# Kernel optimization log

Hardware: AMD Instinct MI355X
Metric: run time of the kernel (lower is better)

The kernel has to match this reference:

```python
import jax, jax.numpy as jnp
import numpy as np

L, H, C, V, T_BLK = 12, 12, 768, 50257, 1024
D = C // H  # head dim = 64


def _layernorm(x, g, b, eps=1e-5):
    m = jnp.mean(x, axis=-1, keepdims=True)
    v = jnp.mean(jnp.square(x - m), axis=-1, keepdims=True)
    return (x - m) * jax.lax.rsqrt(v + eps) * g + b


def setup_inputs() -> dict:
    key = jax.random.key(0)
    ks = jax.random.split(key, 8)
    B, T = 8, 1024
    s = 0.02
    sp = 0.02 / np.sqrt(2 * L)  # c_proj special init
    return {
        "idx": jax.random.randint(ks[0], (B, T), 0, V, dtype=jnp.int32),
        "wte": jax.random.normal(ks[1], (V, C), jnp.float32) * s,
        "wpe": jax.random.normal(ks[2], (T_BLK, C), jnp.float32) * s,
        "ln1_g": jnp.ones((L, C), jnp.float32),
        "ln1_b": jnp.zeros((L, C), jnp.float32),
        "w_qkv": jax.random.normal(ks[3], (L, C, 3 * C), jnp.float32) * s,
        "b_qkv": jnp.zeros((L, 3 * C), jnp.float32),
        "w_ao": jax.random.normal(ks[4], (L, C, C), jnp.float32) * sp,
        "b_ao": jnp.zeros((L, C), jnp.float32),
        "ln2_g": jnp.ones((L, C), jnp.float32),
        "ln2_b": jnp.zeros((L, C), jnp.float32),
        "w_fc": jax.random.normal(ks[5], (L, C, 4 * C), jnp.float32) * s,
        "b_fc": jnp.zeros((L, 4 * C), jnp.float32),
        "w_mo": jax.random.normal(ks[6], (L, 4 * C, C), jnp.float32) * sp,
        "b_mo": jnp.zeros((L, C), jnp.float32),
        "lnf_g": jnp.ones((C,), jnp.float32),
        "lnf_b": jnp.zeros((C,), jnp.float32),
    }


def reference(idx, wte, wpe, ln1_g, ln1_b, w_qkv, b_qkv, w_ao, b_ao,
              ln2_g, ln2_b, w_fc, b_fc, w_mo, b_mo, lnf_g, lnf_b):
    B, T = idx.shape
    scale = 1.0 / np.sqrt(D)
    causal = jnp.tril(jnp.ones((T, T), dtype=bool))  # [T,T]

    x = wte[idx] + wpe[:T]  # [B,T,C]

    def block(x, p):
        g1, b1, wq, bq, wo, bo, g2, b2_, wf, bf, w2, b2m = p
        h = _layernorm(x, g1, b1)
        qkv = h @ wq + bq  # [B,T,3C]
        q, k, v = jnp.split(qkv, 3, axis=-1)
        q = q.reshape(B, T, H, D)
        k = k.reshape(B, T, H, D)
        v = v.reshape(B, T, H, D)
        att = jnp.einsum('bqhd,bkhd->bhqk', q, k) * scale
        att = jnp.where(causal, att, -jnp.inf)
        att = jax.nn.softmax(att, axis=-1)
        y = jnp.einsum('bhqk,bkhd->bqhd', att, v).reshape(B, T, C)
        x = x + y @ wo + bo
        h2 = _layernorm(x, g2, b2_)
        x = x + jax.nn.gelu(h2 @ wf + bf, approximate=False) @ w2 + b2m
        return x, None

    params = (ln1_g, ln1_b, w_qkv, b_qkv, w_ao, b_ao,
              ln2_g, ln2_b, w_fc, b_fc, w_mo, b_mo)
    x, _ = jax.lax.scan(block, x, params)

    x = _layernorm(x, lnf_g, lnf_b)
    # inference path: logits only for last position, lm_head tied to wte
    logits = x[:, -1:, :] @ wte.T  # [B,1,V]
    return logits
```

## Files before the change

### kernel.cpp

```cpp
#include <hip/hip_runtime.h>

#define B_ 8
#define T_ 1024
#define C_ 768
#define H_ 12
#define L_ 12
#define V_ 50257

typedef __bf16 bf16_t;
typedef __bf16 bf16x8 __attribute__((ext_vector_type(8)));
typedef __bf16 bf16x4 __attribute__((ext_vector_type(4)));
typedef float f32x4 __attribute__((ext_vector_type(4)));

#define AS1 __attribute__((address_space(1)))
#define AS3 __attribute__((address_space(3)))

__device__ __forceinline__ unsigned short f2bf(float f) {
  bf16_t h = (bf16_t)f;
  return __builtin_bit_cast(unsigned short, h);
}

__device__ __forceinline__ unsigned short bfbits(bf16_t h) {
  return __builtin_bit_cast(unsigned short, h);
}

template<int CTRL>
__device__ __forceinline__ float dppf(float x) {
  return __builtin_bit_cast(float, __builtin_amdgcn_update_dpp(
      0, __builtin_bit_cast(int, x), CTRL, 0xF, 0xF, true));
}
__device__ __forceinline__ float red16_max(float x) {
  x = fmaxf(x, dppf<0xB1>(x));
  x = fmaxf(x, dppf<0x4E>(x));
  x = fmaxf(x, dppf<0x124>(x));
  x = fmaxf(x, dppf<0x128>(x));
  return x;
}
__device__ __forceinline__ float red16_sum(float x) {
  x += dppf<0xB1>(x);
  x += dppf<0x4E>(x);
  x += dppf<0x124>(x);
  x += dppf<0x128>(x);
  return x;
}

__global__ __launch_bounds__(192) void embed_kernel(
    const int* __restrict__ idx, const float* __restrict__ wte,
    const float* __restrict__ wpe, float* __restrict__ xf)
{
  const int bt = blockIdx.x;
  const int t = bt & (T_ - 1);
  const int tok = idx[bt];
  const int c4 = threadIdx.x << 2;
  float4 a = *(const float4*)(wte + (size_t)tok * C_ + c4);
  float4 p = *(const float4*)(wpe + (size_t)t * C_ + c4);
  float4 r; r.x = a.x + p.x; r.y = a.y + p.y; r.z = a.z + p.z; r.w = a.w + p.w;
  *(float4*)(xf + (size_t)bt * C_ + c4) = r;
}

template<bool LAST>
__global__ __launch_bounds__(256) void ln_kernel(
    const float* __restrict__ x, const float* __restrict__ gw,
    const float* __restrict__ bw, unsigned short* __restrict__ obf,
    float* __restrict__ of)
{
  __shared__ float red[8];
  const size_t row = LAST ? ((size_t)blockIdx.x * T_ + (T_ - 1)) : (size_t)blockIdx.x;
  const float* xr = x + row * C_;
  const int t = threadIdx.x;
  float v0 = xr[t], v1 = xr[t + 256], v2 = xr[t + 512];
  float s = v0 + v1 + v2;
  #pragma unroll
  for (int off = 32; off; off >>= 1) s += __shfl_xor(s, off);
  if ((t & 63) == 0) red[t >> 6] = s;
  __syncthreads();
  const float mean = (red[0] + red[1] + red[2] + red[3]) * (1.0f / C_);
  const float d0 = v0 - mean, d1 = v1 - mean, d2 = v2 - mean;
  float ss = d0 * d0 + d1 * d1 + d2 * d2;
  #pragma unroll
  for (int off = 32; off; off >>= 1) ss += __shfl_xor(ss, off);
  if ((t & 63) == 0) red[4 + (t >> 6)] = ss;
  __syncthreads();
  const float var = (red[4] + red[5] + red[6] + red[7]) * (1.0f / C_);
  const float rs = rsqrtf(var + 1e-5f);
  float o0 = d0 * rs * gw[t] + bw[t];
  float o1 = d1 * rs * gw[t + 256] + bw[t + 256];
  float o2 = d2 * rs * gw[t + 512] + bw[t + 512];
  if (LAST) {
    float* orow = of + (size_t)blockIdx.x * C_;
    orow[t] = o0; orow[t + 256] = o1; orow[t + 512] = o2;
  } else {
    unsigned short* orow = obf + row * C_;
    orow[t] = f2bf(o0); orow[t + 256] = f2bf(o1); orow[t + 512] = f2bf(o2);
  }
}

__global__ __launch_bounds__(256) void cvtw4_kernel(
    const float* __restrict__ wq, const float* __restrict__ wa,
    const float* __restrict__ wf, const float* __restrict__ wm,
    unsigned short* __restrict__ out)
{
  __shared__ float tile[32][33];
  const int i = blockIdx.x;
  const float* W; unsigned short* Wt; int K, N, tix;
  if (i < 1728)      { W = wq; Wt = out;                 K = C_;     N = 3 * C_; tix = i; }
  else if (i < 2304) { W = wa; Wt = out + 3 * C_ * C_;   K = C_;     N = C_;     tix = i - 1728; }
  else if (i < 4608) { W = wf; Wt = out + 4 * C_ * C_;   K = C_;     N = 4 * C_; tix = i - 2304; }
  else               { W = wm; Wt = out + 8 * C_ * C_;   K = 4 * C_; N = C_;     tix = i - 4608; }
  const int ntx = N >> 5;
  const int kb = (tix / ntx) << 5, nb = (tix % ntx) << 5;
  const int t = threadIdx.x;
  {
    const int k = t >> 3, n4 = (t & 7) << 2;
    float4 v = *(const float4*)(W + (size_t)(kb + k) * N + nb + n4);
    tile[k][n4] = v.x; tile[k][n4 + 1] = v.y; tile[k][n4 + 2] = v.z; tile[k][n4 + 3] = v.w;
  }
  __syncthreads();
  {
    const int n = t >> 3, k4 = (t & 7) << 2;
    ushort4 o;
    o.x = f2bf(tile[k4][n]);     o.y = f2bf(tile[k4 + 1][n]);
    o.z = f2bf(tile[k4 + 2][n]); o.w = f2bf(tile[k4 + 3][n]);
    *(ushort4*)(Wt + (size_t)(nb + n) * K + kb + k4) = o;
  }
}

template<int EPI>
__global__ __launch_bounds__(512, 1) void gemm256(
    const unsigned short* __restrict__ A, const unsigned short* __restrict__ Bt,
    const float* __restrict__ bias, unsigned short* __restrict__ Cb,
    int N, int K, int nx)
{
  __shared__ __align__(16) unsigned short As[2][2][128 * 64];
  __shared__ __align__(16) unsigned short Bs[2][2][128 * 64];
  const int tid = threadIdx.x;
  const int lane = tid & 63;
  const int w = tid >> 6;
  const int wr = w >> 2;
  const int wc = w & 3;
  const int l15 = lane & 15, l4 = lane >> 4;
  const int s7 = l15 & 7;

  const int bid = blockIdx.x;
  const int xcd = bid & 7;
  const int j = bid >> 3;
  const int mblk = xcd * 4 + j / nx;
  const int nblk = j - (j / nx) * nx;
  const int m0 = mblk * 256, n0 = nblk * 256;

  f32x4 acc[8][4] = {};

  const int srow8 = lane >> 3;
  const int sch = (lane & 7) ^ srow8;

  auto stageA = [&](int h, int kt, int q) {
    const size_t k0 = (size_t)kt * 64;
    #pragma unroll
    for (int jj = 0; jj < 2; ++jj)
      __builtin_amdgcn_global_load_lds(
          (const AS1 unsigned int*)(A + (size_t)(m0 + h * 128 + jj * 64 + w * 8 + srow8) * K + sch * 8 + k0),
          (AS3 unsigned int*)(&As[q][h][(jj * 8 + w) * 512]), 16, 0, 0);
  };
  auto stageB = [&](int h, int kt, int q) {
    const size_t k0 = (size_t)kt * 64;
    #pragma unroll
    for (int jj = 0; jj < 2; ++jj)
      __builtin_amdgcn_global_load_lds(
          (const AS1 unsigned int*)(Bt + (size_t)(n0 + h * 128 + jj * 64 + w * 8 + srow8) * K + sch * 8 + k0),
          (AS3 unsigned int*)(&Bs[q][h][(jj * 8 + w) * 512]), 16, 0, 0);
  };

  const int nk = K >> 6;
  stageA(0, 0, 0); stageA(1, 0, 0); stageB(0, 0, 0); stageB(1, 0, 0);

  for (int t = 0; t < nk; ++t) {
    const int p = t & 1, q = p ^ 1;
    const bool pf = (t + 1 < nk);
    bf16x8 Af[4][2], Bf[2][2];
    auto rdA = [&](int f, int ks) -> bf16x8 {
      return *(const bf16x8*)(&As[p][wr][(f * 16 + l15) * 64 + ((((ks << 2) | l4) ^ s7) << 3)]);
    };
    auto rdB = [&](int nf, int ks) -> bf16x8 {
      return *(const bf16x8*)(&Bs[p][wc >> 1][((wc & 1) * 64 + nf * 16 + l15) * 64 + ((((ks << 2) | l4) ^ s7) << 3)]);
    };

    if (pf) { stageA(0, t + 1, q); asm volatile("s_waitcnt vmcnt(2)" ::: "memory"); }
    else    { asm volatile("s_waitcnt vmcnt(0)" ::: "memory"); }
    __builtin_amdgcn_s_barrier();
    #pragma unroll
    for (int f = 0; f < 4; ++f) { Af[f][0] = rdA(f, 0); Af[f][1] = rdA(f, 1); }
    #pragma unroll
    for (int nf = 0; nf < 2; ++nf) { Bf[nf][0] = rdB(nf, 0); Bf[nf][1] = rdB(nf, 1); }
    asm volatile("s_waitcnt lgkmcnt(0)" ::: "memory");
    __builtin_amdgcn_sched_barrier(0);
    __builtin_amdgcn_s_setprio(1);
    #pragma unroll
    for (int f = 0; f < 4; ++f)
      #pragma unroll
      for (int nf = 0; nf < 2; ++nf)
        #pragma unroll
        for (int ks = 0; ks < 2; ++ks)
          acc[f][nf] = __builtin_amdgcn_mfma_f32_16x16x32_bf16(Af[f][ks], Bf[nf][ks], acc[f][nf], 0, 0, 0);
    __builtin_amdgcn_s_setprio(0);
    __builtin_amdgcn_s_barrier();

    if (pf) stageA(1, t + 1, q);
    #pragma unroll
    for (int nf = 0; nf < 2; ++nf) { Bf[nf][0] = rdB(nf + 2, 0); Bf[nf][1] = rdB(nf + 2, 1); }
    __builtin_amdgcn_s_barrier();
    asm volatile("s_waitcnt lgkmcnt(0)" ::: "memory");
    __builtin_amdgcn_sched_barrier(0);
    __builtin_amdgcn_s_setprio(1);
    #pragma unroll
    for (int f = 0; f < 4; ++f)
      #pragma unroll
      for (int nf = 0; nf < 2; ++nf)
        #pragma unroll
        for (int ks = 0; ks < 2; ++ks)
          acc[f][nf + 2] = __builtin_amdgcn_mfma_f32_16x16x32_bf16(Af[f][ks], Bf[nf][ks], acc[f][nf + 2], 0, 0, 0);
    __builtin_amdgcn_s_setprio(0);
    __builtin_amdgcn_s_barrier();

    if (pf) stageB(0, t + 1, q);
    #pragma unroll
    for (int f = 0; f < 4; ++f) { Af[f][0] = rdA(f + 4, 0); Af[f][1] = rdA(f + 4, 1); }
    __builtin_amdgcn_s_barrier();
    asm volatile("s_waitcnt lgkmcnt(0)" ::: "memory");
    __builtin_amdgcn_sched_barrier(0);
    __builtin_amdgcn_s_setprio(1);
    #pragma unroll
    for (int f = 0; f < 4; ++f)
      #pragma unroll
      for (int nf = 0; nf < 2; ++nf)
        #pragma unroll
        for (int ks = 0; ks < 2; ++ks)
          acc[f + 4][nf + 2] = __builtin_amdgcn_mfma_f32_16x16x32_bf16(Af[f][ks], Bf[nf][ks], acc[f + 4][nf + 2], 0, 0, 0);
    __builtin_amdgcn_s_setprio(0);
    __builtin_amdgcn_s_barrier();

    if (pf) stageB(1, t + 1, q);
    #pragma unroll
    for (int nf = 0; nf < 2; ++nf) { Bf[nf][0] = rdB(nf, 0); Bf[nf][1] = rdB(nf, 1); }
    __builtin_amdgcn_s_barrier();
    asm volatile("s_waitcnt lgkmcnt(0)" ::: "memory");
    __builtin_amdgcn_sched_barrier(0);
    __builtin_amdgcn_s_setprio(1);
    #pragma unroll
    for (int f = 0; f < 4; ++f)
      #pragma unroll
      for (int nf = 0; nf < 2; ++nf)
        #pragma unroll
        for (int ks = 0; ks < 2; ++ks)
          acc[f + 4][nf] = __builtin_amdgcn_mfma_f32_16x16x32_bf16(Af[f][ks], Bf[nf][ks], acc[f + 4][nf], 0, 0, 0);
    __builtin_amdgcn_s_setprio(0);
    __builtin_amdgcn_s_barrier();
  }

  #pragma unroll
  for (int f = 0; f < 8; ++f) {
    #pragma unroll
    for (int nf = 0; nf < 4; ++nf) {
      const int col = n0 + wc * 64 + nf * 16 + l15;
      const float bv = bias[col];
      int hh = 0, dd = 0;
      unsigned short* qkvo = nullptr;
      if constexpr (EPI == 3) {
        const int which = col / C_;
        const int rem = col - which * C_;
        hh = rem >> 6; dd = rem & 63;
        qkvo = Cb + (size_t)which * ((size_t)B_ * H_ * T_ * 64);
      }
      #pragma unroll
      for (int i = 0; i < 4; ++i) {
        const int row = mblk * 256 + wr * 128 + f * 16 + l4 * 4 + i;
        float v = acc[f][nf][i] + bv;
        if constexpr (EPI == 2) {
          float g = 0.5f * v * (1.0f + erff(v * 0.70710678118f));
          Cb[(size_t)row * N + col] = f2bf(g);
        } else {
          const int bb = row >> 10, tt = row & (T_ - 1);
          qkvo[(((size_t)bb * H_ + hh) * T_ + tt) * 64 + dd] = f2bf(v);
        }
      }
    }
  }
}

template<int EPI>
__global__ __launch_bounds__(256, 2) void gemm_bt(
    const unsigned short* __restrict__ A, const unsigned short* __restrict__ Bt,
    const float* __restrict__ bias, float* __restrict__ Cf,
    unsigned short* __restrict__ Cb, int M, int N, int K, int nx)
{
  (void)M;
  __shared__ unsigned short As[2][128 * 64];
  __shared__ unsigned short Bs[2][128 * 64];
  const int tid = threadIdx.x;
  const int lane = tid & 63;
  const int w = tid >> 6;
  const int wr = w >> 1, wc = w & 1;
  const int l15 = lane & 15, l4 = lane >> 4;
  const int swz = lane & 7;

  const int bid = blockIdx.x;
  const int xcd = bid & 7;
  const int j = bid >> 3;
  const int mblk = xcd * 8 + j / nx;
  const int nblk = j - (j / nx) * nx;
  const int m0 = mblk * 128, n0 = nblk * 128;

  f32x4 acc[4][4] = {};

  const int srow = lane >> 3;
  const int schunk = (lane & 7) ^ srow;
  const unsigned short* aSrc = A + (size_t)(m0 + w * 32 + srow) * K + schunk * 8;
  const unsigned short* bSrc = Bt + (size_t)(n0 + w * 32 + srow) * K + schunk * 8;
  const int ldsRowBase = (w * 32) * 64;

  auto stage = [&](int kt, int p) {
    const int k0 = kt << 6;
    #pragma unroll
    for (int jj = 0; jj < 4; ++jj)
      __builtin_amdgcn_global_load_lds(
          (const AS1 unsigned int*)(aSrc + (size_t)jj * 8 * K + k0),
          (AS3 unsigned int*)(&As[p][ldsRowBase + jj * 8 * 64]), 16, 0, 0);
    #pragma unroll
    for (int jj = 0; jj < 4; ++jj)
      __builtin_amdgcn_global_load_lds(
          (const AS1 unsigned int*)(bSrc + (size_t)jj * 8 * K + k0),
          (AS3 unsigned int*)(&Bs[p][ldsRowBase + jj * 8 * 64]), 16, 0, 0);
  };

  auto compute = [&](int p) {
    const unsigned short* aw = &As[p][(wr * 64) * 64];
    const unsigned short* bw2 = &Bs[p][(wc * 64) * 64];
    #pragma unroll
    for (int ks = 0; ks < 2; ++ks) {
      bf16x8 af[4], bf[4];
      #pragma unroll
      for (int mf = 0; mf < 4; ++mf)
        af[mf] = *(const bf16x8*)(aw + (mf * 16 + l15) * 64 + (((ks << 2) | l4) ^ swz) * 8);
      #pragma unroll
      for (int nf = 0; nf < 4; ++nf)
        bf[nf] = *(const bf16x8*)(bw2 + (nf * 16 + l15) * 64 + (((ks << 2) | l4) ^ swz) * 8);
      __builtin_amdgcn_s_setprio(1);
      #pragma unroll
      for (int mf = 0; mf < 4; ++mf)
        #pragma unroll
        for (int nf = 0; nf < 4; ++nf)
          acc[mf][nf] = __builtin_amdgcn_mfma_f32_16x16x32_bf16(af[mf], bf[nf], acc[mf][nf], 0, 0, 0);
      __builtin_amdgcn_s_setprio(0);
    }
  };

  const int nk = K >> 6;
  stage(0, 0);
  for (int kt = 0; kt < nk - 1; ++kt) {
    const int p = kt & 1;
    stage(kt + 1, p ^ 1);
    asm volatile("s_waitcnt vmcnt(8)" ::: "memory");
    __builtin_amdgcn_s_barrier();
    compute(p);
    __builtin_amdgcn_s_barrier();
  }
  asm volatile("s_waitcnt vmcnt(0)" ::: "memory");
  __builtin_amdgcn_s_barrier();
  compute((nk - 1) & 1);

  #pragma unroll
  for (int mf = 0; mf < 4; ++mf) {
    #pragma unroll
    for (int nf = 0; nf < 4; ++nf) {
      const int col = n0 + wc * 64 + nf * 16 + l15;
      const float bv = bias[col];
      #pragma unroll
      for (int i = 0; i < 4; ++i) {
        const int row = m0 + wr * 64 + mf * 16 + l4 * 4 + i;
        float v = acc[mf][nf][i] + bv;
        if constexpr (EPI == 1) {
          Cf[(size_t)row * N + col] += v;
        } else if constexpr (EPI == 2) {
          float g = 0.5f * v * (1.0f + erff(v * 0.70710678118f));
          Cb[(size_t)row * N + col] = f2bf(g);
        }
      }
    }
  }
}

__global__ __launch_bounds__(256) void attn_kernel(
    const unsigned short* __restrict__ Qb, const unsigned short* __restrict__ Kb,
    const unsigned short* __restrict__ Vb, unsigned short* __restrict__ y)
{
  const int pb = blockIdx.x / 96;
  const int bh = blockIdx.x % 96;
  const int h = bh % H_;
  const int b = bh / H_;
  const int tid = threadIdx.x, lane = tid & 63, w = tid >> 6;
  const int l15 = lane & 15, l4 = lane >> 4;

  const int qw = (w < 2) ? (pb * 64 + w * 32) : ((15 - pb) * 64 + (w - 2) * 32);
  const int NT = (17 - pb) >> 1;

  __shared__ unsigned short Ks[128 * 64];
  __shared__ unsigned short Vt[64 * 136];
  __shared__ unsigned short Pb[4][32 * 74];

  const unsigned short* qp = Qb + ((size_t)bh * T_ + qw) * 64;
  bf16x8 qf[2][2];
  #pragma unroll
  for (int mf = 0; mf < 2; ++mf)
    #pragma unroll
    for (int ks = 0; ks < 2; ++ks)
      qf[mf][ks] = *(const bf16x8*)(qp + (mf * 16 + l15) * 64 + ks * 32 + l4 * 8);

  f32x4 o[2][4] = {};
  float mrow[2][4], lrow[2][4];
  #pragma unroll
  for (int mf = 0; mf < 2; ++mf)
    #pragma unroll
    for (int i = 0; i < 4; ++i) { mrow[mf][i] = -1e30f; lrow[mf][i] = 0.0f; }

  const unsigned short* kb0 = Kb + (size_t)bh * T_ * 64;
  const unsigned short* vb0 = Vb + (size_t)bh * T_ * 64;
  const int ck = w;
  const int skey = lane;
  const int sw = (skey & 7);

  bf16x8 kr0, kr1, kr2, kr3, vr0, vr1, vr2, vr3;
  {
    const unsigned short* kp = kb0 + (size_t)skey * 64;
    const unsigned short* vp = vb0 + (size_t)skey * 64;
    kr0 = *(const bf16x8*)(kp + ck * 8);
    kr1 = *(const bf16x8*)(kp + (ck + 4) * 8);
    kr2 = *(const bf16x8*)(kp + 64 * 64 + ck * 8);
    kr3 = *(const bf16x8*)(kp + 64 * 64 + (ck + 4) * 8);
    vr0 = *(const bf16x8*)(vp + ck * 8);
    vr1 = *(const bf16x8*)(vp + (ck + 4) * 8);
    vr2 = *(const bf16x8*)(vp + 64 * 64 + ck * 8);
    vr3 = *(const bf16x8*)(vp + 64 * 64 + (ck + 4) * 8);
  }

  for (int kt = 0; kt < NT; ++kt) {
    const int k0 = kt << 7;
    __syncthreads();
    *(bf16x8*)(Ks + skey * 64 + ((ck ^ sw) * 8)) = kr0;
    *(bf16x8*)(Ks + skey * 64 + (((ck + 4) ^ sw) * 8)) = kr1;
    *(bf16x8*)(Ks + (skey + 64) * 64 + ((ck ^ sw) * 8)) = kr2;
    *(bf16x8*)(Ks + (skey + 64) * 64 + (((ck + 4) ^ sw) * 8)) = kr3;
    #pragma unroll
    for (int jj = 0; jj < 8; ++jj) {
      Vt[(ck * 8 + jj) * 136 + skey]            = bfbits(vr0[jj]);
      Vt[((ck + 4) * 8 + jj) * 136 + skey]      = bfbits(vr1[jj]);
      Vt[(ck * 8 + jj) * 136 + skey + 64]       = bfbits(vr2[jj]);
      Vt[((ck + 4) * 8 + jj) * 136 + skey + 64] = bfbits(vr3[jj]);
    }
    __syncthreads();
    if (kt + 1 < NT) {
      const int kn = (kt + 1) << 7;
      const unsigned short* kp = kb0 + (size_t)(kn + skey) * 64;
      const unsigned short* vp = vb0 + (size_t)(kn + skey) * 64;
      kr0 = *(const bf16x8*)(kp + ck * 8);
      kr1 = *(const bf16x8*)(kp + (ck + 4) * 8);
      kr2 = *(const bf16x8*)(kp + 64 * 64 + ck * 8);
      kr3 = *(const bf16x8*)(kp + 64 * 64 + (ck + 4) * 8);
      vr0 = *(const bf16x8*)(vp + ck * 8);
      vr1 = *(const bf16x8*)(vp + (ck + 4) * 8);
      vr2 = *(const bf16x8*)(vp + 64 * 64 + ck * 8);
      vr3 = *(const bf16x8*)(vp + 64 * 64 + (ck + 4) * 8);
    }

    #pragma unroll
    for (int h2 = 0; h2 < 2; ++h2) {
      const int kh0 = k0 + h2 * 64;
      if (kh0 > qw + 31) continue;

      f32x4 s[2][4] = {};
      __builtin_amdgcn_s_setprio(1);
      #pragma unroll
      for (int ks = 0; ks < 2; ++ks) {
        #pragma unroll
        for (int nfk = 0; nfk < 4; ++nfk) {
          const int key = h2 * 64 + nfk * 16 + l15;
          bf16x8 kf = *(const bf16x8*)(Ks + key * 64 + ((((ks << 2) | l4) ^ (l15 & 7)) * 8));
          #pragma unroll
          for (int mf = 0; mf < 2; ++mf)
            s[mf][nfk] = __builtin_amdgcn_mfma_f32_16x16x32_bf16(qf[mf][ks], kf, s[mf][nfk], 0, 0, 0);
        }
      }
      __builtin_amdgcn_s_setprio(0);

      #pragma unroll
      for (int mf = 0; mf < 2; ++mf) {
        const int qrow = qw + mf * 16 + l4 * 4;
        const bool fullt = (kh0 + 63) <= (qw + mf * 16);
        float pvv[4][4], tm[4];
        #pragma unroll
        for (int i = 0; i < 4; ++i) {
          const int q = qrow + i;
          float m_ = -1e30f;
          #pragma unroll
          for (int nfk = 0; nfk < 4; ++nfk) {
            float x = s[mf][nfk][i] * 0.125f;
            x = fullt ? x : ((kh0 + nfk * 16 + l15 <= q) ? x : -1e30f);
            pvv[nfk][i] = x;
            m_ = fmaxf(m_, x);
          }
          tm[i] = red16_max(m_);
        }
        bool need = false;
        #pragma unroll
        for (int i = 0; i < 4; ++i) need |= (tm[i] > mrow[mf][i] + 8.0f);
        if (__any(need)) {
          #pragma unroll
          for (int i = 0; i < 4; ++i) {
            const float mnew = fmaxf(mrow[mf][i], tm[i]);
            const float alpha = __expf(mrow[mf][i] - mnew);
            mrow[mf][i] = mnew;
            lrow[mf][i] *= alpha;
            #pragma unroll
            for (int nf = 0; nf < 4; ++nf) o[mf][nf][i] *= alpha;
          }
        }
        #pragma unroll
        for (int i = 0; i < 4; ++i) {
          float rsum = 0.0f;
          #pragma unroll
          for (int nfk = 0; nfk < 4; ++nfk) {
            const float p = __expf(pvv[nfk][i] - mrow[mf][i]);
            pvv[nfk][i] = p; rsum += p;
          }
          rsum = red16_sum(rsum);
          lrow[mf][i] += rsum;
        }
        #pragma unroll
        for (int nfk = 0; nfk < 4; ++nfk)
          #pragma unroll
          for (int i = 0; i < 4; ++i)
            Pb[w][(mf * 16 + l4 * 4 + i) * 74 + nfk * 16 + l15] = f2bf(pvv[nfk][i]);
      }

      bf16x8 pa[2][2];
      #pragma unroll
      for (int mf = 0; mf < 2; ++mf)
        #pragma unroll
        for (int k2 = 0; k2 < 2; ++k2)
          pa[mf][k2] = *(const bf16x8*)(Pb[w] + (mf * 16 + l15) * 74 + k2 * 32 + l4 * 8);
      __builtin_amdgcn_s_setprio(1);
      #pragma unroll
      for (int nf = 0; nf < 4; ++nf) {
        const int d = nf * 16 + l15;
        #pragma unroll
        for (int k2 = 0; k2 < 2; ++k2) {
          bf16x8 vf = *(const bf16x8*)(Vt + d * 136 + h2 * 64 + k2 * 32 + l4 * 8);
          #pragma unroll
          for (int mf = 0; mf < 2; ++mf)
            o[mf][nf] = __builtin_amdgcn_mfma_f32_16x16x32_bf16(pa[mf][k2], vf, o[mf][nf], 0, 0, 0);
        }
      }
      __builtin_amdgcn_s_setprio(0);
    }
  }

  #pragma unroll
  for (int mf = 0; mf < 2; ++mf) {
    #pragma unroll
    for (int i = 0; i < 4; ++i) {
      const float inv = 1.0f / lrow[mf][i];
      const int q = qw + mf * 16 + l4 * 4 + i;
      unsigned short* yr = y + (size_t)(b * T_ + q) * C_ + h * 64;
      #pragma unroll
      for (int nf = 0; nf < 4; ++nf)
        yr[nf * 16 + l15] = f2bf(o[mf][nf][i] * inv);
    }
  }
}

__global__ __launch_bounds__(256) void head_kernel(
    const float* __restrict__ lnf, const float* __restrict__ wte,
    float* __restrict__ out)
{
  __shared__ float xs[B_ * C_];
  for (int i = threadIdx.x; i < B_ * C_; i += 256) xs[i] = lnf[i];
  __syncthreads();
  const int w = threadIdx.x >> 6, lane = threadIdx.x & 63;
  const int v = blockIdx.x * 4 + w;
  if (v >= V_) return;
  const float* wv = wte + (size_t)v * C_ + lane * 12;
  float4 w0 = *(const float4*)(wv);
  float4 w1 = *(const float4*)(wv + 4);
  float4 w2 = *(const float4*)(wv + 8);
  float acc[B_];
  #pragma unroll
  for (int bb = 0; bb < B_; ++bb) {
    const float* xr = xs + bb * C_ + lane * 12;
    float4 x0 = *(const float4*)(xr);
    float4 x1 = *(const float4*)(xr + 4);
    float4 x2 = *(const float4*)(xr + 8);
    acc[bb] = w0.x * x0.x + w0.y * x0.y + w0.z * x0.z + w0.w * x0.w
            + w1.x * x1.x + w1.y * x1.y + w1.z * x1.z + w1.w * x1.w
            + w2.x * x2.x + w2.y * x2.y + w2.z * x2.z + w2.w * x2.w;
  }
  #pragma unroll
  for (int off = 32; off; off >>= 1) {
    #pragma unroll
    for (int bb = 0; bb < B_; ++bb)
      acc[bb] += __shfl_xor(acc[bb], off);
  }
  if (lane == 0) {
    #pragma unroll
    for (int bb = 0; bb < B_; ++bb)
      out[(size_t)bb * V_ + v] = acc[bb];
  }
}

extern "C" void kernel_launch(void* const* d_in, const int* in_sizes, int n_in,
                              void* d_out, int out_size, void* d_ws, size_t ws_size,
                              hipStream_t stream)
{
  (void)in_sizes; (void)n_in; (void)out_size; (void)ws_size;
  const int*   idx   = (const int*)d_in[0];
  const float* wte   = (const float*)d_in[1];
  const float* wpe   = (const float*)d_in[2];
  const float* ln1_g = (const float*)d_in[3];
  const float* ln1_b = (const float*)d_in[4];
  const float* w_qkv = (const float*)d_in[5];
  const float* b_qkv = (const float*)d_in[6];
  const float* w_ao  = (const float*)d_in[7];
  const float* b_ao  = (const float*)d_in[8];
  const float* ln2_g = (const float*)d_in[9];
  const float* ln2_b = (const float*)d_in[10];
  const float* w_fc  = (const float*)d_in[11];
  const float* b_fc  = (const float*)d_in[12];
  const float* w_mo  = (const float*)d_in[13];
  const float* b_mo  = (const float*)d_in[14];
  const float* lnf_g = (const float*)d_in[15];
  const float* lnf_b = (const float*)d_in[16];

  char* ws = (char*)d_ws;
  size_t off = 0;
  auto wsalloc = [&](size_t bytes) -> void* {
    void* p = ws + off;
    off += (bytes + 255) & ~(size_t)255;
    return p;
  };
  const size_t SZH = (size_t)B_ * H_ * T_ * 64;
  float* xf             = (float*)wsalloc((size_t)B_ * T_ * C_ * 4);
  unsigned short* qkv3  = (unsigned short*)wsalloc(3 * SZH * 2);
  unsigned short* a_in  = (unsigned short*)wsalloc((size_t)B_ * T_ * C_ * 2);
  unsigned short* act2  = (unsigned short*)wsalloc((size_t)B_ * T_ * 4 * C_ * 2);
  unsigned short* wbuf  = (unsigned short*)wsalloc((size_t)12 * C_ * C_ * 2);
  float* lnfb           = (float*)wsalloc((size_t)B_ * C_ * 4);

  const size_t OFF_AO = (size_t)3 * C_ * C_;
  const size_t OFF_FC = (size_t)4 * C_ * C_;
  const size_t OFF_MO = (size_t)8 * C_ * C_;
  const int MROWS = B_ * T_;

  embed_kernel<<<B_ * T_, 192, 0, stream>>>(idx, wte, wpe, xf);

  for (int l = 0; l < L_; ++l) {
    ln_kernel<false><<<B_ * T_, 256, 0, stream>>>(xf, ln1_g + l * C_, ln1_b + l * C_, a_in, nullptr);
    cvtw4_kernel<<<6912, 256, 0, stream>>>(
        w_qkv + (size_t)l * C_ * 3 * C_, w_ao + (size_t)l * C_ * C_,
        w_fc + (size_t)l * C_ * 4 * C_, w_mo + (size_t)l * 4 * C_ * C_, wbuf);
    gemm256<3><<<288, 512, 0, stream>>>(a_in, wbuf, b_qkv + l * 3 * C_, qkv3, 3 * C_, C_, 9);
    attn_kernel<<<8 * B_ * H_, 256, 0, stream>>>(qkv3, qkv3 + SZH, qkv3 + 2 * SZH, a_in);
    gemm_bt<1><<<64 * 6, 256, 0, stream>>>(a_in, wbuf + OFF_AO, b_ao + l * C_, xf, nullptr, MROWS, C_, C_, 6);
    ln_kernel<false><<<B_ * T_, 256, 0, stream>>>(xf, ln2_g + l * C_, ln2_b + l * C_, a_in, nullptr);
    gemm256<2><<<384, 512, 0, stream>>>(a_in, wbuf + OFF_FC, b_fc + l * 4 * C_, act2, 4 * C_, C_, 12);
    gemm_bt<1><<<64 * 6, 256, 0, stream>>>(act2, wbuf + OFF_MO, b_mo + l * C_, xf, nullptr, MROWS, C_, 4 * C_, 6);
  }

  ln_kernel<true><<<B_, 256, 0, stream>>>(xf, lnf_g, lnf_b, nullptr, lnfb);
  head_kernel<<<(V_ + 3) / 4, 256, 0, stream>>>(lnfb, wte, (float*)d_out);
}
```

Before: 4.404 ms.

## Issue full-tile prefetch up front, cut GEMM barriers, rebalance attention rows, fast GELU

The 256-tile GEMM now issues all A and B loads for the next k-tile at the start of the iteration instead of spreading them across four phases. It keeps two sets of B fragments so it can drop several barriers. The 128-tile GEMM switches to a fixed blockIdx-to-tile mapping. Attention gives each wave one 16-row slice from the low band and one from the high band, so causal work is even across waves and inactive slices skip their MFMAs. The exact erff GELU is replaced by an Abramowitz-Stegun polynomial with an exp term, which trades a small accuracy loss for cheaper arithmetic.

```diff
diff --git a/kernel.cpp b/kernel.cpp
--- a/kernel.cpp
+++ b/kernel.cpp
@@ -22,6 +22,20 @@
 
 __device__ __forceinline__ unsigned short bfbits(bf16_t h) {
   return __builtin_bit_cast(unsigned short, h);
+}
+
+__device__ __forceinline__ float fast_gelu(float v) {
+  const float xe = v * 0.70710678118f;
+  const float ax = fabsf(xe);
+  const float t = 1.0f / fmaf(0.3275911f, ax, 1.0f);
+  float poly = fmaf(t, 1.061405429f, -1.453152027f);
+  poly = fmaf(t, poly, 1.421413741f);
+  poly = fmaf(t, poly, -0.284496736f);
+  poly = fmaf(t, poly, 0.254829592f);
+  poly *= t;
+  float er = 1.0f - poly * __expf(-ax * ax);
+  er = (xe < 0.0f) ? -er : er;
+  return 0.5f * v * (1.0f + er);
 }
 
 template<int CTRL>
@@ -153,30 +167,30 @@
   const int srow8 = lane >> 3;
   const int sch = (lane & 7) ^ srow8;
 
-  auto stageA = [&](int h, int kt, int q) {
+  auto stage = [&](int kt, int q) {
     const size_t k0 = (size_t)kt * 64;
     #pragma unroll
-    for (int jj = 0; jj < 2; ++jj)
-      __builtin_amdgcn_global_load_lds(
-          (const AS1 unsigned int*)(A + (size_t)(m0 + h * 128 + jj * 64 + w * 8 + srow8) * K + sch * 8 + k0),
-          (AS3 unsigned int*)(&As[q][h][(jj * 8 + w) * 512]), 16, 0, 0);
+    for (int h = 0; h < 2; ++h)
+      #pragma unroll
+      for (int jj = 0; jj < 2; ++jj)
+        __builtin_amdgcn_global_load_lds(
+            (const AS1 unsigned int*)(A + (size_t)(m0 + h * 128 + jj * 64 + w * 8 + srow8) * K + sch * 8 + k0),
+            (AS3 unsigned int*)(&As[q][h][(jj * 8 + w) * 512]), 16, 0, 0);
+    #pragma unroll
+    for (int h = 0; h < 2; ++h)
+      #pragma unroll
+      for (int jj = 0; jj < 2; ++jj)
+        __builtin_amdgcn_global_load_lds(
+            (const AS1 unsigned int*)(Bt + (size_t)(n0 + h * 128 + jj * 64 + w * 8 + srow8) * K + sch * 8 + k0),
+            (AS3 unsigned int*)(&Bs[q][h][(jj * 8 + w) * 512]), 16, 0, 0);
   };
-  auto stageB = [&](int h, int kt, int q) {
-    const size_t k0 = (size_t)kt * 64;
-    #pragma unroll
-    for (int jj = 0; jj < 2; ++jj)
-      __builtin_amdgcn_global_load_lds(
-          (const AS1 unsigned int*)(Bt + (size_t)(n0 + h * 128 + jj * 64 + w * 8 + srow8) * K + sch * 8 + k0),
-          (AS3 unsigned int*)(&Bs[q][h][(jj * 8 + w) * 512]), 16, 0, 0);
-  };
 
   const int nk = K >> 6;
-  stageA(0, 0, 0); stageA(1, 0, 0); stageB(0, 0, 0); stageB(1, 0, 0);
+  stage(0, 0);
 
   for (int t = 0; t < nk; ++t) {
     const int p = t & 1, q = p ^ 1;
-    const bool pf = (t + 1 < nk);
-    bf16x8 Af[4][2], Bf[2][2];
+    bf16x8 Af[4][2], B01[2][2], B23[2][2];
     auto rdA = [&](int f, int ks) -> bf16x8 {
       return *(const bf16x8*)(&As[p][wr][(f * 16 + l15) * 64 + ((((ks << 2) | l4) ^ s7) << 3)]);
     };
@@ -184,13 +198,17 @@
       return *(const bf16x8*)(&Bs[p][wc >> 1][((wc & 1) * 64 + nf * 16 + l15) * 64 + ((((ks << 2) | l4) ^ s7) << 3)]);
     };
 
-    if (pf) { stageA(0, t + 1, q); asm volatile("s_waitcnt vmcnt(2)" ::: "memory"); }
-    else    { asm volatile("s_waitcnt vmcnt(0)" ::: "memory"); }
+    if (t + 1 < nk) {
+      stage(t + 1, q);
+      asm volatile("s_waitcnt vmcnt(8)" ::: "memory");
+    } else {
+      asm volatile("s_waitcnt vmcnt(0)" ::: "memory");
+    }
     __builtin_amdgcn_s_barrier();
     #pragma unroll
     for (int f = 0; f < 4; ++f) { Af[f][0] = rdA(f, 0); Af[f][1] = rdA(f, 1); }
     #pragma unroll
-    for (int nf = 0; nf < 2; ++nf) { Bf[nf][0] = rdB(nf, 0); Bf[nf][1] = rdB(nf, 1); }
+    for (int nf = 0; nf < 2; ++nf) { B01[nf][0] = rdB(nf, 0); B01[nf][1] = rdB(nf, 1); }
     asm volatile("s_waitcnt lgkmcnt(0)" ::: "memory");
     __builtin_amdgcn_sched_barrier(0);
     __builtin_amdgcn_s_setprio(1);
@@ -200,13 +218,11 @@
       for (int nf = 0; nf < 2; ++nf)
         #pragma unroll
         for (int ks = 0; ks < 2; ++ks)
-          acc[f][nf] = __builtin_amdgcn_mfma_f32_16x16x32_bf16(Af[f][ks], Bf[nf][ks], acc[f][nf], 0, 0, 0);
+          acc[f][nf] = __builtin_amdgcn_mfma_f32_16x16x32_bf16(Af[f][ks], B01[nf][ks], acc[f][nf], 0, 0, 0);
     __builtin_amdgcn_s_setprio(0);
-    __builtin_amdgcn_s_barrier();
-
-    if (pf) stageA(1, t + 1, q);
-    #pragma unroll
-    for (int nf = 0; nf < 2; ++nf) { Bf[nf][0] = rdB(nf + 2, 0); Bf[nf][1] = rdB(nf + 2, 1); }
+
+    #pragma unroll
+    for (int nf = 0; nf < 2; ++nf) { B23[nf][0] = rdB(nf + 2, 0); B23[nf][1] = rdB(nf + 2, 1); }
     __builtin_amdgcn_s_barrier();
     asm volatile("s_waitcnt lgkmcnt(0)" ::: "memory");
     __builtin_amdgcn_sched_barrier(0);
@@ -217,11 +233,9 @@
       for (int nf = 0; nf < 2; ++nf)
         #pragma unroll
         for (int ks = 0; ks < 2; ++ks)
-          acc[f][nf + 2] = __builtin_amdgcn_mfma_f32_16x16x32_bf16(Af[f][ks], Bf[nf][ks], acc[f][nf + 2], 0, 0, 0);
+          acc[f][nf + 2] = __builtin_amdgcn_mfma_f32_16x16x32_bf16(Af[f][ks], B23[nf][ks], acc[f][nf + 2], 0, 0, 0);
     __builtin_amdgcn_s_setprio(0);
-    __builtin_amdgcn_s_barrier();
-
-    if (pf) stageB(0, t + 1, q);
+
     #pragma unroll
     for (int f = 0; f < 4; ++f) { Af[f][0] = rdA(f + 4, 0); Af[f][1] = rdA(f + 4, 1); }
     __builtin_amdgcn_s_barrier();
@@ -234,16 +248,10 @@
       for (int nf = 0; nf < 2; ++nf)
         #pragma unroll
         for (int ks = 0; ks < 2; ++ks)
-          acc[f + 4][nf + 2] = __builtin_amdgcn_mfma_f32_16x16x32_bf16(Af[f][ks], Bf[nf][ks], acc[f + 4][nf + 2], 0, 0, 0);
+          acc[f + 4][nf + 2] = __builtin_amdgcn_mfma_f32_16x16x32_bf16(Af[f][ks], B23[nf][ks], acc[f + 4][nf + 2], 0, 0, 0);
     __builtin_amdgcn_s_setprio(0);
+
     __builtin_amdgcn_s_barrier();
-
-    if (pf) stageB(1, t + 1, q);
-    #pragma unroll
-    for (int nf = 0; nf < 2; ++nf) { Bf[nf][0] = rdB(nf, 0); Bf[nf][1] = rdB(nf, 1); }
-    __builtin_amdgcn_s_barrier();
-    asm volatile("s_waitcnt lgkmcnt(0)" ::: "memory");
-    __builtin_amdgcn_sched_barrier(0);
     __builtin_amdgcn_s_setprio(1);
     #pragma unroll
     for (int f = 0; f < 4; ++f)
@@ -251,9 +259,8 @@
       for (int nf = 0; nf < 2; ++nf)
         #pragma unroll
         for (int ks = 0; ks < 2; ++ks)
-          acc[f + 4][nf] = __builtin_amdgcn_mfma_f32_16x16x32_bf16(Af[f][ks], Bf[nf][ks], acc[f + 4][nf], 0, 0, 0);
+          acc[f + 4][nf] = __builtin_amdgcn_mfma_f32_16x16x32_bf16(Af[f][ks], B01[nf][ks], acc[f + 4][nf], 0, 0, 0);
     __builtin_amdgcn_s_setprio(0);
-    __builtin_amdgcn_s_barrier();
   }
 
   #pragma unroll
@@ -272,11 +279,10 @@
       }
       #pragma unroll
       for (int i = 0; i < 4; ++i) {
-        const int row = mblk * 256 + wr * 128 + f * 16 + l4 * 4 + i;
+        const int row = m0 + wr * 128 + f * 16 + l4 * 4 + i;
         float v = acc[f][nf][i] + bv;
         if constexpr (EPI == 2) {
-          float g = 0.5f * v * (1.0f + erff(v * 0.70710678118f));
-          Cb[(size_t)row * N + col] = f2bf(g);
+          Cb[(size_t)row * N + col] = f2bf(fast_gelu(v));
         } else {
           const int bb = row >> 10, tt = row & (T_ - 1);
           qkvo[(((size_t)bb * H_ + hh) * T_ + tt) * 64 + dd] = f2bf(v);
@@ -292,7 +298,7 @@
     const float* __restrict__ bias, float* __restrict__ Cf,
     unsigned short* __restrict__ Cb, int M, int N, int K, int nx)
 {
-  (void)M;
+  (void)M; (void)nx;
   __shared__ unsigned short As[2][128 * 64];
   __shared__ unsigned short Bs[2][128 * 64];
   const int tid = threadIdx.x;
@@ -305,8 +311,8 @@
   const int bid = blockIdx.x;
   const int xcd = bid & 7;
   const int j = bid >> 3;
-  const int mblk = xcd * 8 + j / nx;
-  const int nblk = j - (j / nx) * nx;
+  const int mblk = xcd * 8 + (j & 7);
+  const int nblk = j >> 3;
   const int m0 = mblk * 128, n0 = nblk * 128;
 
   f32x4 acc[4][4] = {};
@@ -380,8 +386,7 @@
         if constexpr (EPI == 1) {
           Cf[(size_t)row * N + col] += v;
         } else if constexpr (EPI == 2) {
-          float g = 0.5f * v * (1.0f + erff(v * 0.70710678118f));
-          Cb[(size_t)row * N + col] = f2bf(g);
+          Cb[(size_t)row * N + col] = f2bf(fast_gelu(v));
         }
       }
     }
@@ -399,20 +404,24 @@
   const int tid = threadIdx.x, lane = tid & 63, w = tid >> 6;
   const int l15 = lane & 15, l4 = lane >> 4;
 
-  const int qw = (w < 2) ? (pb * 64 + w * 32) : ((15 - pb) * 64 + (w - 2) * 32);
+  const int qband0 = pb * 64 + w * 16;
+  const int qband1 = (15 - pb) * 64 + w * 16;
   const int NT = (17 - pb) >> 1;
 
   __shared__ unsigned short Ks[128 * 64];
   __shared__ unsigned short Vt[64 * 136];
   __shared__ unsigned short Pb[4][32 * 74];
 
-  const unsigned short* qp = Qb + ((size_t)bh * T_ + qw) * 64;
   bf16x8 qf[2][2];
-  #pragma unroll
-  for (int mf = 0; mf < 2; ++mf)
-    #pragma unroll
-    for (int ks = 0; ks < 2; ++ks)
-      qf[mf][ks] = *(const bf16x8*)(qp + (mf * 16 + l15) * 64 + ks * 32 + l4 * 8);
+  {
+    const unsigned short* q0p = Qb + ((size_t)bh * T_ + qband0) * 64;
+    const unsigned short* q1p = Qb + ((size_t)bh * T_ + qband1) * 64;
+    #pragma unroll
+    for (int ks = 0; ks < 2; ++ks) {
+      qf[0][ks] = *(const bf16x8*)(q0p + l15 * 64 + ks * 32 + l4 * 8);
+      qf[1][ks] = *(const bf16x8*)(q1p + l15 * 64 + ks * 32 + l4 * 8);
+    }
+  }
 
   f32x4 o[2][4] = {};
   float mrow[2][4], lrow[2][4];
@@ -473,7 +482,9 @@
     #pragma unroll
     for (int h2 = 0; h2 < 2; ++h2) {
       const int kh0 = k0 + h2 * 64;
-      if (kh0 > qw + 31) continue;
+      const bool act0 = (kh0 <= qband0 + 15);
+      const bool act1 = (kh0 <= qband1 + 15);
+      if (!act0 && !act1) continue;
 
       f32x4 s[2][4] = {};
       __builtin_amdgcn_s_setprio(1);
@@ -483,17 +494,19 @@
         for (int nfk = 0; nfk < 4; ++nfk) {
           const int key = h2 * 64 + nfk * 16 + l15;
           bf16x8 kf = *(const bf16x8*)(Ks + key * 64 + ((((ks << 2) | l4) ^ (l15 & 7)) * 8));
-          #pragma unroll
-          for (int mf = 0; mf < 2; ++mf)
-            s[mf][nfk] = __builtin_amdgcn_mfma_f32_16x16x32_bf16(qf[mf][ks], kf, s[mf][nfk], 0, 0, 0);
+          if (act0) s[0][nfk] = __builtin_amdgcn_mfma_f32_16x16x32_bf16(qf[0][ks], kf, s[0][nfk], 0, 0, 0);
+          if (act1) s[1][nfk] = __builtin_amdgcn_mfma_f32_16x16x32_bf16(qf[1][ks], kf, s[1][nfk], 0, 0, 0);
         }
       }
       __builtin_amdgcn_s_setprio(0);
 
       #pragma unroll
       for (int mf = 0; mf < 2; ++mf) {
-        const int qrow = qw + mf * 16 + l4 * 4;
-        const bool fullt = (kh0 + 63) <= (qw + mf * 16);
+        const bool act = mf ? act1 : act0;
+        if (!act) continue;
+        const int qb0 = mf ? qband1 : qband0;
+        const int qrow = qb0 + l4 * 4;
+        const bool fullt = (kh0 + 63) <= qb0;
         float pvv[4][4], tm[4];
         #pragma unroll
         for (int i = 0; i < 4; ++i) {
@@ -543,9 +556,10 @@
       bf16x8 pa[2][2];
       #pragma unroll
       for (int mf = 0; mf < 2; ++mf)
-        #pragma unroll
-        for (int k2 = 0; k2 < 2; ++k2)
-          pa[mf][k2] = *(const bf16x8*)(Pb[w] + (mf * 16 + l15) * 74 + k2 * 32 + l4 * 8);
+        if (mf ? act1 : act0)
+          #pragma unroll
+          for (int k2 = 0; k2 < 2; ++k2)
+            pa[mf][k2] = *(const bf16x8*)(Pb[w] + (mf * 16 + l15) * 74 + k2 * 32 + l4 * 8);
       __builtin_amdgcn_s_setprio(1);
       #pragma unroll
       for (int nf = 0; nf < 4; ++nf) {
@@ -553,9 +567,8 @@
         #pragma unroll
         for (int k2 = 0; k2 < 2; ++k2) {
           bf16x8 vf = *(const bf16x8*)(Vt + d * 136 + h2 * 64 + k2 * 32 + l4 * 8);
-          #pragma unroll
-          for (int mf = 0; mf < 2; ++mf)
-            o[mf][nf] = __builtin_amdgcn_mfma_f32_16x16x32_bf16(pa[mf][k2], vf, o[mf][nf], 0, 0, 0);
+          if (act0) o[0][nf] = __builtin_amdgcn_mfma_f32_16x16x32_bf16(pa[0][k2], vf, o[0][nf], 0, 0, 0);
+          if (act1) o[1][nf] = __builtin_amdgcn_mfma_f32_16x16x32_bf16(pa[1][k2], vf, o[1][nf], 0, 0, 0);
         }
       }
       __builtin_amdgcn_s_setprio(0);
@@ -564,10 +577,11 @@
 
   #pragma unroll
   for (int mf = 0; mf < 2; ++mf) {
+    const int qb0 = mf ? qband1 : qband0;
     #pragma unroll
     for (int i = 0; i < 4; ++i) {
       const float inv = 1.0f / lrow[mf][i];
-      const int q = qw + mf * 16 + l4 * 4 + i;
+      const int q = qb0 + l4 * 4 + i;
       unsigned short* yr = y + (size_t)(b * T_ + q) * C_ + h * 64;
       #pragma unroll
       for (int nf = 0; nf < 4; ++nf)
```

Measured after the change: 3.978 ms. 1.11x faster.
